# Kernel optimization log

Measured on AMD Instinct MI355X. Metric: run time of the kernel, lower is better.

The kernel has to match this reference:

```python
import jax, jax.numpy as jnp
import numpy as np

N_NODES = 20000
IN_CH = 128
OUT_CH = 128
HEADS = 1
OB_DIM = 4
N_STEP = 32           # = HEADS*OUT_CH*8 // 32
D_PE = 16             # 32 - HEADS*16
N_EDGES = 256000


def setup_inputs() -> dict:
    key = jax.random.key(0)
    ks = jax.random.split(key, 9)
    x = jax.random.normal(ks[0], (N_NODES, IN_CH), jnp.float32)
    p_t = jax.random.normal(ks[1], (N_STEP, D_PE), jnp.float32)
    edge_index = jax.random.randint(ks[2], (2, N_EDGES), 0, N_NODES, jnp.int32)
    edge_weights = jax.random.uniform(ks[3], (N_EDGES,), jnp.float32)
    # Linear params (PyTorch default init: U(-1/sqrt(fan_in), 1/sqrt(fan_in)))
    s = 1.0 / np.sqrt(IN_CH)
    lin_value_w = jax.random.uniform(ks[4], (IN_CH, HEADS * OUT_CH), jnp.float32, -s, s)
    lin_value_b = jax.random.uniform(ks[5], (HEADS * OUT_CH,), jnp.float32, -s, s)
    inc_w = jax.random.uniform(ks[6], (IN_CH, HEADS * OUT_CH * 8), jnp.float32, -s, s)
    inc_b = jax.random.uniform(ks[7], (HEADS * OUT_CH * 8,), jnp.float32, -s, s)
    g = np.sqrt(6.0 / (N_NODES + HEADS * 16))  # glorot
    map_weights = jax.random.uniform(ks[8], (N_NODES, HEADS * 16), jnp.float32, -g, g)
    return {"x": x, "p_t": p_t, "edge_index": edge_index, "edge_weights": edge_weights,
            "lin_value_w": lin_value_w, "lin_value_b": lin_value_b,
            "inc_w": inc_w, "inc_b": inc_b, "map_weights": map_weights}


def _segment_softmax(gamma, index, num_segments):
    # PyG-style softmax over edges grouped by destination index, per column
    m = jax.ops.segment_max(gamma, index, num_segments=num_segments)     # [N, D]
    num = jnp.exp(gamma - m[index])
    den = jax.ops.segment_sum(num, index, num_segments=num_segments)    # [N, D]
    return num / den[index]


def reference(x, p_t, edge_index, edge_weights, lin_value_w, lin_value_b,
              inc_w, inc_b, map_weights):
    src = edge_index[0]   # x_j side
    dst = edge_index[1]   # x_i side (flow source_to_target)
    n_step = p_t.shape[0]
    E = src.shape[0]

    x_i = x[dst]                                             # [E, in]
    # h_W = increase_dim(x_i).view(E, n_step, 32)
    h_W = (x_i @ inc_w + inc_b).reshape(E, n_step, 32)       # [E, T, 32]
    w_v = map_weights[dst]                                   # [E, 16]
    # beta = mean(h_W * cat([w_v, p_t], -1), -1) computed without materializing aa
    beta = (jnp.einsum('etk,ek->et', h_W[:, :, :16], w_v)
            + jnp.einsum('etk,tk->et', h_W[:, :, 16:], p_t)) / 32.0   # [E, T]

    gamma = beta * edge_weights[:, None]                     # [E, T]
    gamma = jnp.repeat(gamma, OB_DIM, axis=-1)               # [E, T*ob_dim] = [E, H*out]
    all_edge_weights = jnp.mean(gamma, axis=1)               # [E]

    K = int(E * 0.5)
    _, top_idx = jax.lax.top_k(all_edge_weights, K)          # top-K edges
    gamma = gamma[top_idx]                                   # [K, H*out]
    x_i = x_i[top_idx]                                       # [K, in]
    # NOTE: the module re-points aggregation index to edge_index[0] (source)
    index = src[top_idx]                                     # [K]

    gamma = _segment_softmax(gamma, index, N_NODES)          # [K, H*out]

    v = jax.nn.relu(x_i @ lin_value_w + lin_value_b)         # [K, H*out]
    msg = (v.reshape(K, HEADS, OUT_CH)
           * gamma.reshape(K, HEADS, OUT_CH))                # [K, H, out]

    out = jax.ops.segment_sum(msg.reshape(K, HEADS * OUT_CH), index,
                              num_segments=N_NODES)          # scatter-add
    return out                                               # [N, H*out]
```

## Files before the change

kernel.cpp:

```cpp
#include <hip/hip_runtime.h>

#define NN 20000
#define IC 128
#define OC 128
#define NSTEP 32
#define NE 256000
#define KSEL 128000
#define NB 79
#define CH 64
#define ECH 4000
#define RND 16
#define HPW 10000
#define CANDCAP 65536
#define NQCOL 704

struct SelState {
  unsigned long long prefix;
  unsigned r;
  unsigned selc;
  unsigned tiec;
  unsigned done[8];
};

typedef __attribute__((ext_vector_type(16))) float f16v;

__global__ void k_init(const float* __restrict__ p_t, const float* __restrict__ lin_w,
                       const float* __restrict__ lin_b,
                       const float* __restrict__ inc_w, const float* __restrict__ inc_b,
                       float* __restrict__ Wq,
                       double* __restrict__ Ud, double* __restrict__ ubd,
                       unsigned* __restrict__ hist, SelState* st) {
  int i = blockIdx.x * blockDim.x + threadIdx.x;
  if (i < 33 * NQCOL) {
    int k4 = i / NQCOL, col = i - k4 * NQCOL;
    float4 o;
    float* ov = (float*)&o;
    for (int jj = 0; jj < 4; ++jj) {
      int k = 4 * k4 + jj;
      float v = 0.f;
      if (col < 512) {
        int t = col >> 4, c = col & 15;
        if (k < 128) v = inc_w[k * 1024 + t * 32 + c];
        else if (k == 128) v = inc_b[t * 32 + c];
      } else if (col < 544) {
        int t = col - 512;
        if (k < 128) {
          float a = 0.f;
          for (int q = 0; q < 16; ++q) a += inc_w[k * 1024 + t * 32 + 16 + q] * p_t[t * 16 + q];
          v = a;
        } else if (k == 128) {
          float a = 0.f;
          for (int q = 0; q < 16; ++q) a += inc_b[t * 32 + 16 + q] * p_t[t * 16 + q];
          v = a;
        }
      } else if (col < 672) {
        int c = col - 544;
        if (k < 128) v = lin_w[k * OC + c];
        else if (k == 128) v = lin_b[c];
      }
      ov[jj] = v;
    }
    ((float4*)Wq)[i] = o;
    return;
  }
  i -= 33 * NQCOL;
  if (i < 17 * IC) {
    int c = i >> 7, k = i & 127;
    double a = 0.0;
    if (c < 16) {
      for (int t = 0; t < NSTEP; ++t) a += (double)inc_w[k * 1024 + t * 32 + c];
    } else {
      for (int t = 0; t < NSTEP; ++t)
        for (int q = 0; q < 16; ++q)
          a += (double)inc_w[k * 1024 + t * 32 + 16 + q] * (double)p_t[t * 16 + q];
    }
    Ud[c * IC + k] = a;
    return;
  }
  i -= 17 * IC;
  if (i < 17) {
    double a = 0.0;
    if (i < 16) {
      for (int t = 0; t < NSTEP; ++t) a += (double)inc_b[t * 32 + i];
    } else {
      for (int t = 0; t < NSTEP; ++t)
        for (int q = 0; q < 16; ++q)
          a += (double)inc_b[t * 32 + 16 + q] * (double)p_t[t * 16 + q];
    }
    ubd[i] = a;
    return;
  }
  i -= 17;
  if (i < 512) { hist[i] = 0u; return; }
  i -= 512;
  if (i == 0) {
    st->prefix = 0ull; st->r = KSEL; st->selc = 0u; st->tiec = 0u;
    for (int p = 0; p < 8; ++p) st->done[p] = 0u;
  }
}

#define FMA4(WV, BASE)                                                                        \
  acc[BASE+0] = fmaf(xf.x, WV[0],  fmaf(xf.y, WV[1],  fmaf(xf.z, WV[2],  fmaf(xf.w, WV[3],  acc[BASE+0])))); \
  acc[BASE+1] = fmaf(xf.x, WV[4],  fmaf(xf.y, WV[5],  fmaf(xf.z, WV[6],  fmaf(xf.w, WV[7],  acc[BASE+1])))); \
  acc[BASE+2] = fmaf(xf.x, WV[8],  fmaf(xf.y, WV[9],  fmaf(xf.z, WV[10], fmaf(xf.w, WV[11], acc[BASE+2])))); \
  acc[BASE+3] = fmaf(xf.x, WV[12], fmaf(xf.y, WV[13], fmaf(xf.z, WV[14], fmaf(xf.w, WV[15], acc[BASE+3]))));

__global__ __launch_bounds__(256) void k_node(
    const float* __restrict__ x, const float* __restrict__ mw,
    const float* __restrict__ Wq,
    float* __restrict__ beta, float* __restrict__ V) {
  __shared__ float4 xl[64 * 32];
  int tid = threadIdx.x;
  int g = blockIdx.x;
  int s = blockIdx.y;
  int n0 = g * 64;
  int nvalid = NN - n0; if (nvalid > 64) nvalid = 64;

  for (int i = tid; i < 64 * 32; i += 256) {
    int mm = i >> 5, k4 = i & 31;
    float4 v = make_float4(0.f, 0.f, 0.f, 0.f);
    if (mm < nvalid) v = ((const float4*)(x + (size_t)(n0 + mm) * IC))[k4];
    xl[(mm << 5) + ((k4 + mm) & 31)] = v;
  }
  int m = tid & 63;
  int j = __builtin_amdgcn_readfirstlane(threadIdx.x >> 6);
  __syncthreads();

  for (int r = 0; r < 2; ++r) {
    int u = s * 8 + j + r * 4;
    if (u < 32) {
      float mwr[16];
      {
        int mm = (m < nvalid) ? m : 0;
        const float4* mp = (const float4*)(mw + (size_t)(n0 + mm) * 16);
#pragma unroll
        for (int i = 0; i < 4; ++i) {
          float4 t4 = mp[i];
          mwr[4 * i] = t4.x; mwr[4 * i + 1] = t4.y; mwr[4 * i + 2] = t4.z; mwr[4 * i + 3] = t4.w;
        }
      }
      const f16v*   wb = (const f16v*)Wq + (u << 2);
      const float4* wp = (const float4*)Wq + (512 + u);
      float acc[16], accp;
      {
        const f16v* wkb = wb + 32 * 176;
        f16v b0 = wkb[0], b1 = wkb[1], b2 = wkb[2], b3 = wkb[3];
#pragma unroll
        for (int c = 0; c < 4; ++c) {
          acc[c] = b0[4 * c]; acc[4 + c] = b1[4 * c];
          acc[8 + c] = b2[4 * c]; acc[12 + c] = b3[4 * c];
        }
        accp = wp[32 * NQCOL].x;
      }
      f16v w0 = wb[0], w1 = wb[1], w2 = wb[2], w3 = wb[3];
      float4 pw = wp[0];
      for (int k4 = 0; k4 < 32; ++k4) {
        f16v nw0, nw1, nw2, nw3; float4 npw;
        if (k4 < 31) {
          const f16v* wn = wb + (k4 + 1) * 176;
          nw0 = wn[0]; nw1 = wn[1]; nw2 = wn[2]; nw3 = wn[3];
          npw = wp[(k4 + 1) * NQCOL];
        }
        float4 xf = xl[(m << 5) + ((k4 + m) & 31)];
        FMA4(w0, 0) FMA4(w1, 4) FMA4(w2, 8) FMA4(w3, 12)
        accp = fmaf(xf.x, pw.x, fmaf(xf.y, pw.y, fmaf(xf.z, pw.z, fmaf(xf.w, pw.w, accp))));
        if (k4 < 31) { w0 = nw0; w1 = nw1; w2 = nw2; w3 = nw3; pw = npw; }
      }
      float bs = accp;
#pragma unroll
      for (int c = 0; c < 16; ++c) bs = fmaf(acc[c], mwr[c], bs);
      if (m < nvalid) beta[(size_t)(n0 + m) * NSTEP + u] = bs * (1.f / 32.f);
    } else {
      int vg = u - 32;
      int vc0 = vg << 4;
      const f16v* wb = (const f16v*)Wq + 136 + (vg << 2);
      float acc[16];
      {
        const f16v* wkb = wb + 32 * 176;
        f16v b0 = wkb[0], b1 = wkb[1], b2 = wkb[2], b3 = wkb[3];
#pragma unroll
        for (int c = 0; c < 4; ++c) {
          acc[c] = b0[4 * c]; acc[4 + c] = b1[4 * c];
          acc[8 + c] = b2[4 * c]; acc[12 + c] = b3[4 * c];
        }
      }
      f16v w0 = wb[0], w1 = wb[1], w2 = wb[2], w3 = wb[3];
      for (int k4 = 0; k4 < 32; ++k4) {
        f16v nw0, nw1, nw2, nw3;
        if (k4 < 31) {
          const f16v* wn = wb + (k4 + 1) * 176;
          nw0 = wn[0]; nw1 = wn[1]; nw2 = wn[2]; nw3 = wn[3];
        }
        float4 xf = xl[(m << 5) + ((k4 + m) & 31)];
        FMA4(w0, 0) FMA4(w1, 4) FMA4(w2, 8) FMA4(w3, 12)
        if (k4 < 31) { w0 = nw0; w1 = nw1; w2 = nw2; w3 = nw3; }
      }
      if (m < nvalid) {
        float* vout = V + (size_t)(n0 + m) * OC + vc0;
#pragma unroll
        for (int q = 0; q < 4; ++q) {
          float4 o;
          o.x = fmaxf(acc[4 * q], 0.f);     o.y = fmaxf(acc[4 * q + 1], 0.f);
          o.z = fmaxf(acc[4 * q + 2], 0.f); o.w = fmaxf(acc[4 * q + 3], 0.f);
          ((float4*)vout)[q] = o;
        }
      }
    }
  }
}

__global__ __launch_bounds__(256) void k_s64(
    const float* __restrict__ x, const float* __restrict__ mw,
    const double* __restrict__ Ud, const double* __restrict__ ubd,
    double* __restrict__ s64) {
  int tid = blockIdx.x * 256 + threadIdx.x;
  int m = tid >> 4, c = tid & 15;
  if (m >= NN) return;
  const float*  xr  = x + (size_t)m * IC;
  const double* uc  = Ud + c * IC;
  const double* u16 = Ud + 16 * IC;
  double a = 0.0, a16 = 0.0;
  for (int k = 0; k < IC; k += 4) {
    float4 xv = *(const float4*)(xr + k);
    a   = fma((double)xv.x, uc[k],      a);
    a   = fma((double)xv.y, uc[k + 1],  a);
    a   = fma((double)xv.z, uc[k + 2],  a);
    a   = fma((double)xv.w, uc[k + 3],  a);
    a16 = fma((double)xv.x, u16[k],     a16);
    a16 = fma((double)xv.y, u16[k + 1], a16);
    a16 = fma((double)xv.z, u16[k + 2], a16);
    a16 = fma((double)xv.w, u16[k + 3], a16);
  }
  double part = (a + ubd[c]) * (double)mw[m * 16 + c];
#pragma unroll
  for (int d = 1; d < 16; d <<= 1) part += __shfl_xor(part, d, 64);
  if (c == 0) s64[m] = (part + a16 + ubd[16]) * (1.0 / 1024.0);
}

__global__ void k_keysel(const int* __restrict__ ei, const float* __restrict__ ew,
                         const double* __restrict__ s64,
                         unsigned long long* __restrict__ keys,
                         unsigned* __restrict__ hist, SelState* st) {
  __shared__ unsigned h[256], suf[256];
  __shared__ int last;
  int tid = threadIdx.x;
  h[tid] = 0u;
  if (tid == 0) last = 0;
  __syncthreads();
  for (int e = blockIdx.x * 256 + tid; e < NE; e += gridDim.x * 256) {
    int d = ei[NE + e];
    double v = s64[d] * (double)ew[e];
    unsigned long long u = (unsigned long long)__double_as_longlong(v);
    u = (u & 0x8000000000000000ull) ? ~u : (u | 0x8000000000000000ull);
    keys[e] = u;
    atomicAdd(&h[(unsigned)(u >> 56)], 1u);
  }
  __syncthreads();
  if (h[tid]) atomicAdd(&hist[tid], h[tid]);
  __threadfence();
  __syncthreads();
  if (tid == 0) {
    if (atomicAdd(&st->done[0], 1u) == gridDim.x - 1) last = 1;
  }
  __syncthreads();
  if (!last) return;
  unsigned c = atomicAdd(&hist[tid], 0u);
  suf[tid] = c;
  __syncthreads();
  for (int d = 1; d < 256; d <<= 1) {
    unsigned v = (tid + d < 256) ? suf[tid + d] : 0u;
    __syncthreads();
    suf[tid] += v;
    __syncthreads();
  }
  unsigned r = st->r;
  unsigned exc = suf[tid] - c;
  if (exc < r && exc + c >= r) {
    st->prefix = (unsigned long long)tid;
    st->r = r - exc;
  }
}

__global__ void k_radix1(const unsigned long long* __restrict__ keys,
                         unsigned* __restrict__ hist, SelState* st) {
  __shared__ unsigned h[256], suf[256];
  __shared__ int last;
  int tid = threadIdx.x;
  h[tid] = 0u;
  if (tid == 0) last = 0;
  unsigned long long pref = st->prefix;
  __syncthreads();
  unsigned* hp = hist + 256;
  for (int e = blockIdx.x * 256 + tid; e < NE; e += gridDim.x * 256) {
    unsigned long long k = keys[e];
    if ((k >> 56) == pref)
      atomicAdd(&h[(unsigned)((k >> 48) & 255ull)], 1u);
  }
  __syncthreads();
  if (h[tid]) atomicAdd(&hp[tid], h[tid]);
  __threadfence();
  __syncthreads();
  if (tid == 0) {
    if (atomicAdd(&st->done[1], 1u) == gridDim.x - 1) last = 1;
  }
  __syncthreads();
  if (!last) return;
  unsigned c = atomicAdd(&hp[tid], 0u);
  suf[tid] = c;
  __syncthreads();
  for (int d = 1; d < 256; d <<= 1) {
    unsigned v = (tid + d < 256) ? suf[tid + d] : 0u;
    __syncthreads();
    suf[tid] += v;
    __syncthreads();
  }
  unsigned r = st->r;
  unsigned exc = suf[tid] - c;
  if (exc < r && exc + c >= r) {
    st->prefix = (st->prefix << 8) | (unsigned long long)tid;
    st->r = r - exc;
  }
}

__global__ void k_candsel(const unsigned long long* __restrict__ keys,
                          SelState* st,
                          unsigned long long* __restrict__ flags,
                          unsigned long long* __restrict__ candk, int* __restrict__ cande) {
  __shared__ unsigned h[256], suf[256];
  __shared__ unsigned long long spref;
  __shared__ unsigned sr;
  __shared__ int last;
  int tid = threadIdx.x;
  if (tid == 0) last = 0;
  unsigned P16 = (unsigned)st->prefix;
  for (int e = blockIdx.x * 256 + tid; e < NE; e += gridDim.x * 256) {
    unsigned long long k = keys[e];
    unsigned t16 = (unsigned)(k >> 48);
    unsigned long long bal = __ballot(t16 > P16);
    if ((tid & 63) == 0) flags[e >> 6] = bal;
    if (t16 == P16) {
      unsigned pos = atomicAdd(&st->tiec, 1u);
      if (pos < CANDCAP) { candk[pos] = k; cande[pos] = e; }
    }
  }
  __threadfence();
  __syncthreads();
  if (tid == 0) {
    if (atomicAdd(&st->done[2], 1u) == gridDim.x - 1) last = 1;
  }
  __syncthreads();
  if (!last) return;
  unsigned C = atomicAdd(&st->tiec, 0u); if (C > CANDCAP) C = CANDCAP;
  if (tid == 0) { spref = (unsigned long long)P16; sr = st->r; }
  __syncthreads();
  for (int p = 2; p < 8; ++p) {
    h[tid] = 0u;
    __syncthreads();
    int shift = 56 - 8 * p;
    unsigned long long pf = spref;
    unsigned r = sr;
    for (unsigned i = tid; i < C; i += 256) {
      unsigned long long k = candk[i];
      if ((k >> (shift + 8)) == pf) atomicAdd(&h[(unsigned)((k >> shift) & 255ull)], 1u);
    }
    __syncthreads();
    suf[tid] = h[tid];
    __syncthreads();
    for (int d = 1; d < 256; d <<= 1) {
      unsigned v = (tid + d < 256) ? suf[tid + d] : 0u;
      __syncthreads();
      suf[tid] += v;
      __syncthreads();
    }
    unsigned exc = suf[tid] - h[tid];
    if (exc < r && exc + h[tid] >= r) {
      spref = (pf << 8) | (unsigned long long)tid;
      sr = r - exc;
    }
    __syncthreads();
  }
  unsigned long long T = spref;
  unsigned needed = sr;
  for (unsigned i = tid; i < C; i += 256) {
    unsigned long long k = candk[i];
    int e2 = cande[i];
    bool take = false;
    if (k > T) take = true;
    else if (k == T) {
      unsigned rank = 0;
      for (unsigned q = 0; q < C; ++q)
        rank += (candk[q] == T && cande[q] < e2) ? 1u : 0u;
      take = (rank < needed);
    }
    if (take) atomicOr(&flags[e2 >> 6], 1ull << (e2 & 63));
  }
}

__global__ __launch_bounds__(256) void k_count1(const int* __restrict__ ei,
                                                const unsigned long long* __restrict__ flags,
                                                unsigned* __restrict__ hpart) {
  __shared__ unsigned hp[HPW];
  int tid = threadIdx.x;
  for (int i = tid; i < HPW; i += 256) hp[i] = 0u;
  __syncthreads();
  int base = blockIdx.x * ECH;
  int lim = base + ECH; if (lim > NE) lim = NE;
  for (int k0 = 0; k0 < RND; k0 += 4) {
    int nn[4]; bool tk[4];
#pragma unroll
    for (int q = 0; q < 4; ++q) {
      int e = base + tid + (k0 + q) * 256;
      bool valid = e < lim;
      unsigned long long w = valid ? flags[e >> 6] : 0ull;
      nn[q] = valid ? ei[e] : 0;
      tk[q] = valid && ((w >> (e & 63)) & 1ull);
    }
#pragma unroll
    for (int q = 0; q < 4; ++q)
      if (tk[q]) atomicAdd(&hp[nn[q] >> 1], 1u << ((nn[q] & 1) * 16));
  }
  __syncthreads();
  unsigned* dst = hpart + (size_t)blockIdx.x * HPW;
  for (int i = tid; i < HPW; i += 256) dst[i] = hp[i];
}

__global__ void k_prefA(const unsigned* __restrict__ hpart,
                        unsigned short* __restrict__ hoffl,
                        unsigned* __restrict__ cnt, unsigned* __restrict__ bsum,
                        unsigned* __restrict__ bbase, unsigned* __restrict__ offar,
                        SelState* st) {
  __shared__ unsigned sd[256];
  __shared__ int last;
  int tid = threadIdx.x;
  if (tid == 0) last = 0;
  int n = blockIdx.x * 256 + tid;
  unsigned tot = 0u;
  if (n < NN) {
    int half = (n & 1) * 16;
    int wi = n >> 1;
#pragma unroll 4
    for (int b = 0; b < CH; ++b) {
      hoffl[(size_t)b * NN + n] = (unsigned short)tot;
      tot += (hpart[(size_t)b * HPW + wi] >> half) & 0xFFFFu;
    }
    cnt[n] = tot;
  }
  sd[tid] = (n < NN) ? tot : 0u;
  __syncthreads();
  for (int s = 128; s > 0; s >>= 1) {
    if (tid < s) sd[tid] += sd[tid + s];
    __syncthreads();
  }
  if (tid == 0) bsum[blockIdx.x] = sd[0];
  __threadfence();
  __syncthreads();
  if (tid == 0) {
    if (atomicAdd(&st->done[3], 1u) == gridDim.x - 1) last = 1;
  }
  __syncthreads();
  if (!last) return;
  unsigned v = (tid < NB) ? bsum[tid] : 0u;
  sd[tid] = v;
  __syncthreads();
  for (int d = 1; d < 256; d <<= 1) {
    unsigned u = (tid >= d) ? sd[tid - d] : 0u;
    __syncthreads();
    sd[tid] += u;
    __syncthreads();
  }
  if (tid < NB) bbase[tid] = sd[tid] - v;
  if (tid == NB - 1) offar[NN] = sd[tid];
}

__global__ void k_prefB(const unsigned* __restrict__ cnt, const unsigned* __restrict__ bbase,
                        unsigned* __restrict__ offar) {
  __shared__ unsigned sd[256];
  int tid = threadIdx.x;
  int n = blockIdx.x * 256 + tid;
  unsigned v = (n < NN) ? cnt[n] : 0u;
  sd[tid] = v;
  __syncthreads();
  for (int d = 1; d < 256; d <<= 1) {
    unsigned u = (tid >= d) ? sd[tid - d] : 0u;
    __syncthreads();
    sd[tid] += u;
    __syncthreads();
  }
  if (n < NN) offar[n] = bbase[blockIdx.x] + sd[tid] - v;
}

__global__ __launch_bounds__(256) void k_scatterC(const int* __restrict__ ei,
                                                  const unsigned long long* __restrict__ flags,
                                                  const unsigned* __restrict__ offar,
                                                  const unsigned short* __restrict__ hoffl,
                                                  int* __restrict__ csr) {
  __shared__ unsigned rel[HPW];
  int tid = threadIdx.x;
  for (int i = tid; i < HPW; i += 256) rel[i] = 0u;
  __syncthreads();
  int base = blockIdx.x * ECH;
  int lim = base + ECH; if (lim > NE) lim = NE;
  const unsigned short* hl = hoffl + (size_t)blockIdx.x * NN;
  for (int k0 = 0; k0 < RND; k0 += 4) {
    int nn[4]; bool tk[4]; unsigned hb4[4];
#pragma unroll
    for (int q = 0; q < 4; ++q) {
      int e = base + tid + (k0 + q) * 256;
      bool valid = e < lim;
      unsigned long long w = valid ? flags[e >> 6] : 0ull;
      tk[q] = valid && ((w >> (e & 63)) & 1ull);
      nn[q] = valid ? ei[e] : 0;
      hb4[q] = tk[q] ? (offar[nn[q]] + (unsigned)hl[nn[q]]) : 0u;
    }
#pragma unroll
    for (int q = 0; q < 4; ++q) {
      if (tk[q]) {
        int half = (nn[q] & 1) * 16;
        unsigned old = atomicAdd(&rel[nn[q] >> 1], 1u << half);
        unsigned r = (old >> half) & 0xFFFFu;
        unsigned pos = hb4[q] + r;
        if (pos < KSEL) csr[pos] = base + tid + (k0 + q) * 256;
      }
    }
  }
}

__global__ __launch_bounds__(128) void k_out(
    const int* __restrict__ ei, const float* __restrict__ ew,
    const float* __restrict__ beta, const float* __restrict__ V,
    const unsigned* __restrict__ offar, const int* __restrict__ csr,
    float* __restrict__ out) {
  __shared__ float B[32][NSTEP];
  __shared__ float m[NSTEP], den[NSTEP], scale[NSTEP];
  __shared__ int dl[32];
  __shared__ float ewl[32];
  int n = blockIdx.x, tid = threadIdx.x;
  unsigned beg = offar[n], end = offar[n + 1];
  if (end > (unsigned)KSEL) end = KSEL;
  if (beg > end) beg = end;
  if (tid < NSTEP) { m[tid] = -INFINITY; den[tid] = 0.f; }
  float acc = 0.f;
  int c = tid, tq = tid >> 2;
  __syncthreads();

  for (unsigned cb = beg; cb < end; cb += 32u) {
    unsigned ce = end - cb; if (ce > 32u) ce = 32u;
    if (tid < (int)ce) {
      int e = csr[cb + tid];
      dl[tid] = ei[NE + e];
      ewl[tid] = ew[e];
    }
    __syncthreads();
    for (int idx = tid; idx < (int)ce * NSTEP; idx += 128) {
      int el = idx >> 5, t = idx & 31;
      B[el][t] = beta[(size_t)dl[el] * NSTEP + t] * ewl[el];
    }
    __syncthreads();
    if (tid < NSTEP) {
      int t = tid;
      float mc = -INFINITY;
      for (int el = 0; el < (int)ce; ++el) mc = fmaxf(mc, B[el][t]);
      float mnew = fmaxf(m[t], mc);
      float sc = expf(m[t] - mnew);
      float s = 0.f;
      for (int el = 0; el < (int)ce; ++el) {
        float g = expf(B[el][t] - mnew);
        B[el][t] = g;
        s += g;
      }
      den[t] = den[t] * sc + s;
      m[t] = mnew;
      scale[t] = sc;
    }
    __syncthreads();
    acc *= scale[tq];
    for (int el = 0; el < (int)ce; ++el)
      acc += V[(size_t)dl[el] * OC + c] * B[el][tq];
    __syncthreads();
  }
  float d = den[tq];
  out[(size_t)n * OC + c] = (d > 0.f) ? acc / d : 0.f;
}

extern "C" void kernel_launch(void* const* d_in, const int* in_sizes, int n_in,
                              void* d_out, int out_size, void* d_ws, size_t ws_size,
                              hipStream_t stream) {
  const float* x     = (const float*)d_in[0];
  const float* p_t   = (const float*)d_in[1];
  const int*   ei    = (const int*)d_in[2];
  const float* ew    = (const float*)d_in[3];
  const float* lin_w = (const float*)d_in[4];
  const float* lin_b = (const float*)d_in[5];
  const float* inc_w = (const float*)d_in[6];
  const float* inc_b = (const float*)d_in[7];
  const float* mw    = (const float*)d_in[8];
  float* out = (float*)d_out;

  char* w = (char*)d_ws;
  size_t off = 0;
  auto alloc = [&](size_t b) -> void* {
    void* p = w + off;
    off += (b + 511) & ~(size_t)511;
    return p;
  };
  float*  Wq    = (float*)alloc((size_t)33 * NQCOL * 4 * 4);
  double* Ud    = (double*)alloc((size_t)17 * IC * 8);
  double* ubd   = (double*)alloc(17 * 8);
  float*  beta  = (float*)alloc((size_t)NN * NSTEP * 4);
  double* s64   = (double*)alloc((size_t)NN * 8);
  float*  V     = (float*)alloc((size_t)NN * OC * 4);
  unsigned long long* keys  = (unsigned long long*)alloc((size_t)NE * 8);
  unsigned long long* flags = (unsigned long long*)alloc((size_t)(NE / 64) * 8);
  unsigned long long* candk = (unsigned long long*)alloc((size_t)CANDCAP * 8);
  int*      cande  = (int*)alloc((size_t)CANDCAP * 4);
  unsigned* hpart  = (unsigned*)alloc((size_t)CH * HPW * 4);
  unsigned short* hoffl = (unsigned short*)alloc((size_t)CH * NN * 2);
  unsigned* cnt    = (unsigned*)alloc((size_t)NN * 4);
  unsigned* offar  = (unsigned*)alloc((size_t)(NN + 1) * 4);
  int*      csr    = (int*)alloc((size_t)KSEL * 4);
  unsigned* hist   = (unsigned*)alloc(512 * 4);
  unsigned* bsum   = (unsigned*)alloc(NB * 4);
  unsigned* bbase  = (unsigned*)alloc(NB * 4);
  SelState* st     = (SelState*)alloc(sizeof(SelState));
  if (off > ws_size) return;

  int init_threads = 33 * NQCOL + 17 * IC + 17 + 512 + 1;
  k_init<<<(init_threads + 255) / 256, 256, 0, stream>>>(p_t, lin_w, lin_b, inc_w, inc_b,
                                                         Wq, Ud, ubd, hist, st);
  k_node<<<dim3((NN + 63) / 64, 5), 256, 0, stream>>>(x, mw, Wq, beta, V);
  k_s64<<<(NN * 16 + 255) / 256, 256, 0, stream>>>(x, mw, Ud, ubd, s64);
  k_keysel<<<256, 256, 0, stream>>>(ei, ew, s64, keys, hist, st);
  k_radix1<<<256, 256, 0, stream>>>(keys, hist, st);
  k_candsel<<<256, 256, 0, stream>>>(keys, st, flags, candk, cande);
  k_count1<<<CH, 256, 0, stream>>>(ei, flags, hpart);
  k_prefA<<<NB, 256, 0, stream>>>(hpart, hoffl, cnt, bsum, bbase, offar, st);
  k_prefB<<<NB, 256, 0, stream>>>(cnt, bbase, offar);
  k_scatterC<<<CH, 256, 0, stream>>>(ei, flags, offar, hoffl, csr);
  k_out<<<NN, 128, 0, stream>>>(ei, ew, beta, V, offar, csr, out);
}
```

Before: 326.2 us.

## Unroll node GEMM loop by two, tile s64 in LDS, enlarge selection grids

The node-projection inner loops are unrolled by two, with two k-slices of weights prefetched per iteration to expose more memory-level parallelism. k_s64 now stages the double-precision projection matrix and a 16-node tile of x in shared memory (padded rows) and spreads the 17th-column dot product across the 16 lanes instead of having every lane repeat it. The edge key-selection kernels launch one block per 256 edges rather than a fixed 256 blocks. The unroll raises register pressure, and the larger grids add per-block atomics and histogram flushes.

```diff
diff --git a/kernel.cpp b/kernel.cpp
--- a/kernel.cpp
+++ b/kernel.cpp
@@ -152,19 +152,35 @@
         }
         accp = wp[32 * NQCOL].x;
       }
-      f16v w0 = wb[0], w1 = wb[1], w2 = wb[2], w3 = wb[3];
-      float4 pw = wp[0];
-      for (int k4 = 0; k4 < 32; ++k4) {
-        f16v nw0, nw1, nw2, nw3; float4 npw;
-        if (k4 < 31) {
-          const f16v* wn = wb + (k4 + 1) * 176;
-          nw0 = wn[0]; nw1 = wn[1]; nw2 = wn[2]; nw3 = wn[3];
-          npw = wp[(k4 + 1) * NQCOL];
-        }
-        float4 xf = xl[(m << 5) + ((k4 + m) & 31)];
-        FMA4(w0, 0) FMA4(w1, 4) FMA4(w2, 8) FMA4(w3, 12)
-        accp = fmaf(xf.x, pw.x, fmaf(xf.y, pw.y, fmaf(xf.z, pw.z, fmaf(xf.w, pw.w, accp))));
-        if (k4 < 31) { w0 = nw0; w1 = nw1; w2 = nw2; w3 = nw3; pw = npw; }
+      f16v a0 = wb[0], a1 = wb[1], a2 = wb[2], a3 = wb[3];
+      float4 pa = wp[0];
+      f16v c0 = wb[176], c1 = wb[177], c2 = wb[178], c3 = wb[179];
+      float4 pc = wp[NQCOL];
+      for (int k4 = 0; k4 < 32; k4 += 2) {
+        f16v na0, na1, na2, na3, nc0, nc1, nc2, nc3;
+        float4 npa, npc;
+        if (k4 < 30) {
+          const f16v* wn = wb + (k4 + 2) * 176;
+          na0 = wn[0]; na1 = wn[1]; na2 = wn[2]; na3 = wn[3];
+          npa = wp[(k4 + 2) * NQCOL];
+          const f16v* wm2 = wb + (k4 + 3) * 176;
+          nc0 = wm2[0]; nc1 = wm2[1]; nc2 = wm2[2]; nc3 = wm2[3];
+          npc = wp[(k4 + 3) * NQCOL];
+        }
+        {
+          float4 xf = xl[(m << 5) + ((k4 + m) & 31)];
+          FMA4(a0, 0) FMA4(a1, 4) FMA4(a2, 8) FMA4(a3, 12)
+          accp = fmaf(xf.x, pa.x, fmaf(xf.y, pa.y, fmaf(xf.z, pa.z, fmaf(xf.w, pa.w, accp))));
+        }
+        {
+          float4 xf = xl[(m << 5) + ((k4 + 1 + m) & 31)];
+          FMA4(c0, 0) FMA4(c1, 4) FMA4(c2, 8) FMA4(c3, 12)
+          accp = fmaf(xf.x, pc.x, fmaf(xf.y, pc.y, fmaf(xf.z, pc.z, fmaf(xf.w, pc.w, accp))));
+        }
+        if (k4 < 30) {
+          a0 = na0; a1 = na1; a2 = na2; a3 = na3; pa = npa;
+          c0 = nc0; c1 = nc1; c2 = nc2; c3 = nc3; pc = npc;
+        }
       }
       float bs = accp;
 #pragma unroll
@@ -184,16 +200,28 @@
           acc[8 + c] = b2[4 * c]; acc[12 + c] = b3[4 * c];
         }
       }
-      f16v w0 = wb[0], w1 = wb[1], w2 = wb[2], w3 = wb[3];
-      for (int k4 = 0; k4 < 32; ++k4) {
-        f16v nw0, nw1, nw2, nw3;
-        if (k4 < 31) {
-          const f16v* wn = wb + (k4 + 1) * 176;
-          nw0 = wn[0]; nw1 = wn[1]; nw2 = wn[2]; nw3 = wn[3];
-        }
-        float4 xf = xl[(m << 5) + ((k4 + m) & 31)];
-        FMA4(w0, 0) FMA4(w1, 4) FMA4(w2, 8) FMA4(w3, 12)
-        if (k4 < 31) { w0 = nw0; w1 = nw1; w2 = nw2; w3 = nw3; }
+      f16v a0 = wb[0], a1 = wb[1], a2 = wb[2], a3 = wb[3];
+      f16v c0 = wb[176], c1 = wb[177], c2 = wb[178], c3 = wb[179];
+      for (int k4 = 0; k4 < 32; k4 += 2) {
+        f16v na0, na1, na2, na3, nc0, nc1, nc2, nc3;
+        if (k4 < 30) {
+          const f16v* wn = wb + (k4 + 2) * 176;
+          na0 = wn[0]; na1 = wn[1]; na2 = wn[2]; na3 = wn[3];
+          const f16v* wm2 = wb + (k4 + 3) * 176;
+          nc0 = wm2[0]; nc1 = wm2[1]; nc2 = wm2[2]; nc3 = wm2[3];
+        }
+        {
+          float4 xf = xl[(m << 5) + ((k4 + m) & 31)];
+          FMA4(a0, 0) FMA4(a1, 4) FMA4(a2, 8) FMA4(a3, 12)
+        }
+        {
+          float4 xf = xl[(m << 5) + ((k4 + 1 + m) & 31)];
+          FMA4(c0, 0) FMA4(c1, 4) FMA4(c2, 8) FMA4(c3, 12)
+        }
+        if (k4 < 30) {
+          a0 = na0; a1 = na1; a2 = na2; a3 = na3;
+          c0 = nc0; c1 = nc1; c2 = nc2; c3 = nc3;
+        }
       }
       if (m < nvalid) {
         float* vout = V + (size_t)(n0 + m) * OC + vc0;
@@ -213,28 +241,47 @@
     const float* __restrict__ x, const float* __restrict__ mw,
     const double* __restrict__ Ud, const double* __restrict__ ubd,
     double* __restrict__ s64) {
-  int tid = blockIdx.x * 256 + threadIdx.x;
+  __shared__ double udl[17 * 130];
+  __shared__ float4 xs[16 * 32];
+  int tid = threadIdx.x;
+  for (int i = tid; i < 17 * IC; i += 256) {
+    int cc = i >> 7, kk = i & 127;
+    udl[cc * 130 + kk] = Ud[i];
+  }
+  int n0 = blockIdx.x * 16;
+  for (int i = tid; i < 16 * 32; i += 256) {
+    int mm = i >> 5, k4 = i & 31;
+    int n = n0 + mm;
+    xs[i] = (n < NN) ? ((const float4*)(x + (size_t)n * IC))[k4]
+                     : make_float4(0.f, 0.f, 0.f, 0.f);
+  }
+  __syncthreads();
   int m = tid >> 4, c = tid & 15;
-  if (m >= NN) return;
-  const float*  xr  = x + (size_t)m * IC;
-  const double* uc  = Ud + c * IC;
-  const double* u16 = Ud + 16 * IC;
+  int n = n0 + m;
+  const double* uc  = udl + c * 130;
+  const double* u16 = udl + 16 * 130;
   double a = 0.0, a16 = 0.0;
-  for (int k = 0; k < IC; k += 4) {
-    float4 xv = *(const float4*)(xr + k);
-    a   = fma((double)xv.x, uc[k],      a);
-    a   = fma((double)xv.y, uc[k + 1],  a);
-    a   = fma((double)xv.z, uc[k + 2],  a);
-    a   = fma((double)xv.w, uc[k + 3],  a);
-    a16 = fma((double)xv.x, u16[k],     a16);
-    a16 = fma((double)xv.y, u16[k + 1], a16);
-    a16 = fma((double)xv.z, u16[k + 2], a16);
-    a16 = fma((double)xv.w, u16[k + 3], a16);
-  }
-  double part = (a + ubd[c]) * (double)mw[m * 16 + c];
+  for (int k4 = 0; k4 < 32; ++k4) {
+    float4 xv = xs[(m << 5) + k4];
+    a = fma((double)xv.x, uc[4 * k4],     a);
+    a = fma((double)xv.y, uc[4 * k4 + 1], a);
+    a = fma((double)xv.z, uc[4 * k4 + 2], a);
+    a = fma((double)xv.w, uc[4 * k4 + 3], a);
+  }
+#pragma unroll
+  for (int q = 0; q < 2; ++q) {
+    int k4 = 2 * c + q;
+    float4 xv = xs[(m << 5) + k4];
+    a16 = fma((double)xv.x, u16[4 * k4],     a16);
+    a16 = fma((double)xv.y, u16[4 * k4 + 1], a16);
+    a16 = fma((double)xv.z, u16[4 * k4 + 2], a16);
+    a16 = fma((double)xv.w, u16[4 * k4 + 3], a16);
+  }
+  int nm = (n < NN) ? n : 0;
+  double part = (a + ubd[c]) * (double)mw[(size_t)nm * 16 + c] + a16;
 #pragma unroll
   for (int d = 1; d < 16; d <<= 1) part += __shfl_xor(part, d, 64);
-  if (c == 0) s64[m] = (part + a16 + ubd[16]) * (1.0 / 1024.0);
+  if (c == 0 && n < NN) s64[n] = (part + ubd[16]) * (1.0 / 1024.0);
 }
 
 __global__ void k_keysel(const int* __restrict__ ei, const float* __restrict__ ew,
@@ -628,10 +675,10 @@
   k_init<<<(init_threads + 255) / 256, 256, 0, stream>>>(p_t, lin_w, lin_b, inc_w, inc_b,
                                                          Wq, Ud, ubd, hist, st);
   k_node<<<dim3((NN + 63) / 64, 5), 256, 0, stream>>>(x, mw, Wq, beta, V);
-  k_s64<<<(NN * 16 + 255) / 256, 256, 0, stream>>>(x, mw, Ud, ubd, s64);
-  k_keysel<<<256, 256, 0, stream>>>(ei, ew, s64, keys, hist, st);
-  k_radix1<<<256, 256, 0, stream>>>(keys, hist, st);
-  k_candsel<<<256, 256, 0, stream>>>(keys, st, flags, candk, cande);
+  k_s64<<<(NN + 15) / 16, 256, 0, stream>>>(x, mw, Ud, ubd, s64);
+  k_keysel<<<NE / 256, 256, 0, stream>>>(ei, ew, s64, keys, hist, st);
+  k_radix1<<<NE / 256, 256, 0, stream>>>(keys, hist, st);
+  k_candsel<<<NE / 256, 256, 0, stream>>>(keys, st, flags, candk, cande);
   k_count1<<<CH, 256, 0, stream>>>(ei, flags, hpart);
   k_prefA<<<NB, 256, 0, stream>>>(hpart, hoffl, cnt, bsum, bbase, offar, st);
   k_prefB<<<NB, 256, 0, stream>>>(cnt, bbase, offar);
```

Result: slower. 742.4 us (+127.6%).
